# Optimization experiments

Measured on AMD Instinct MI355X. Metric: run time of the kernel, lower is better.

## Reference

```python
import jax, jax.numpy as jnp
import numpy as np

B, T, N, F = 32, 24, 1024, 2   # batch, seq_len, num_adj, num_feature
HID = 32                       # opt['hidden_dim']
U = HID // 2                   # rnn_units = 16
TF = 31                        # opt['time_feature']


def setup_inputs():
    key = jax.random.key(0)
    ks = jax.random.split(key, 40)
    def nrm(k, shape):
        return jax.random.normal(k, shape, dtype=jnp.float32) * 0.05
    inp = {}
    inp['recent_data'] = nrm(ks[0], (B, T, N, F))
    inp['trend_data'] = nrm(ks[1], (B, T, F))
    # normalized adjacency-like matrix (non-negative, row mass ~1)
    inp['sub_graph'] = jax.random.uniform(ks[2], (B, N, N), dtype=jnp.float32) * (2.0 / N)
    inp['time_feature'] = nrm(ks[3], (B, TF))
    i = 4
    for layer, insz in ((1, F + U), (2, U + U)):
        for g in 'ruc':
            inp[f'gru{layer}_{g}W'] = nrm(ks[i], (U, insz)); i += 1
            inp[f'gru{layer}_{g}b'] = jnp.zeros((U,), jnp.float32)
    for l, insz in ((0, F), (1, HID)):
        inp[f'lstm_Wih{l}'] = nrm(ks[i], (4 * HID, insz)); i += 1
        inp[f'lstm_Whh{l}'] = nrm(ks[i], (4 * HID, HID)); i += 1
        inp[f'lstm_bih{l}'] = jnp.zeros((4 * HID,), jnp.float32)
        inp[f'lstm_bhh{l}'] = jnp.zeros((4 * HID,), jnp.float32)
    inp['ff_W'] = nrm(ks[i], (HID, TF)); i += 1
    inp['ff_b'] = jnp.zeros((HID,), jnp.float32)
    inp['gcn_W'] = nrm(ks[i], (F, int(HID * 2.5))); i += 1
    inp['gcn_b'] = jnp.zeros((F,), jnp.float32)
    return inp


def _gcn(x, A, W, b, act):
    # x: (B,N,in), A: (B,N,N) -> act(fc(A @ x)): (B,N,out)
    return act(jnp.einsum('bij,bjf->bif', A, x) @ W.T + b)


def _gru_cell(x, h, A, rW, rb, uW, ub, cW, cb):
    xh = jnp.concatenate([x, h], axis=-1)
    r = _gcn(xh, A, rW, rb, jax.nn.sigmoid)
    u = _gcn(xh, A, uW, ub, jax.nn.sigmoid)
    c = _gcn(jnp.concatenate([x, r * h], axis=-1), A, cW, cb, jnp.tanh)
    return u * h + (1.0 - u) * c


def _lstm_layer(xs, Wih, Whh, bih, bhh):
    # xs: (T, B, in) -> hidden sequence (T, B, H); PyTorch gate order i,f,g,o
    H = Whh.shape[1]
    z = jnp.zeros((xs.shape[1], H), xs.dtype)
    def step(carry, x_t):
        h, c = carry
        g = x_t @ Wih.T + h @ Whh.T + bih + bhh
        i, f, gg, o = jnp.split(g, 4, axis=-1)
        c = jax.nn.sigmoid(f) * c + jax.nn.sigmoid(i) * jnp.tanh(gg)
        h = jax.nn.sigmoid(o) * jnp.tanh(c)
        return (h, c), h
    _, hs = jax.lax.scan(step, (z, z), xs)
    return hs


def _forward(recent_data, trend_data, sub_graph, time_feature,
             gru1_rW, gru1_rb, gru1_uW, gru1_ub, gru1_cW, gru1_cb,
             gru2_rW, gru2_rb, gru2_uW, gru2_ub, gru2_cW, gru2_cb,
             lstm_Wih0, lstm_Whh0, lstm_bih0, lstm_bhh0,
             lstm_Wih1, lstm_Whh1, lstm_bih1, lstm_bhh1,
             ff_W, ff_b, gcn_W, gcn_b):
    b, t, n, _ = recent_data.shape
    u = gru1_rW.shape[0]
    h0 = jnp.zeros((b, n, u), recent_data.dtype)
    # 2-layer GCGRU encoder over time (only final output/state is used)
    def step(carry, x_t):
        h1, h2 = carry
        h1 = _gru_cell(x_t, h1, sub_graph, gru1_rW, gru1_rb, gru1_uW, gru1_ub, gru1_cW, gru1_cb)
        h2 = _gru_cell(h1, h2, sub_graph, gru2_rW, gru2_rb, gru2_uW, gru2_ub, gru2_cW, gru2_cb)
        return (h1, h2), None
    (h1, h2), _ = jax.lax.scan(step, (h0, h0), jnp.swapaxes(recent_data, 0, 1))
    recent = h2  # (B, N, U)
    # 2-layer LSTM on trend_data; take last timestep hidden
    xs = jnp.swapaxes(trend_data, 0, 1)  # (T, B, F)
    hs = _lstm_layer(xs, lstm_Wih0, lstm_Whh0, lstm_bih0, lstm_bhh0)
    hs = _lstm_layer(hs, lstm_Wih1, lstm_Whh1, lstm_bih1, lstm_bhh1)
    trend = jnp.broadcast_to(hs[-1][:, None, :], (b, n, hs.shape[-1]))
    feat = jax.nn.relu(time_feature @ ff_W.T + ff_b)
    feat = jnp.broadcast_to(feat[:, None, :], (b, n, feat.shape[-1]))
    combined = jnp.concatenate([recent, trend, feat], axis=-1)  # (B, N, 2.5*HID)
    return _gcn(combined, sub_graph, gcn_W, gcn_b, jnp.tanh)  # (B, N, F)


def reference(recent_data, trend_data, sub_graph, time_feature,
              gru1_rW, gru1_rb, gru1_uW, gru1_ub, gru1_cW, gru1_cb,
              gru2_rW, gru2_rb, gru2_uW, gru2_ub, gru2_cW, gru2_cb,
              lstm_Wih0, lstm_Whh0, lstm_bih0, lstm_bhh0,
              lstm_Wih1, lstm_Whh1, lstm_bih1, lstm_bhh1,
              ff_W, ff_b, gcn_W, gcn_b):
    return _forward(recent_data, trend_data, sub_graph, time_feature,
                    gru1_rW, gru1_rb, gru1_uW, gru1_ub, gru1_cW, gru1_cb,
                    gru2_rW, gru2_rb, gru2_uW, gru2_ub, gru2_cW, gru2_cb,
                    lstm_Wih0, lstm_Whh0, lstm_bih0, lstm_bhh0,
                    lstm_Wih1, lstm_Whh1, lstm_bih1, lstm_bhh1,
                    ff_W, ff_b, gcn_W, gcn_b)
```

## Files before the change

### kernel.cpp

```cpp
#include <hip/hip_runtime.h>
#include <cmath>
#include <stdint.h>

#define BB 32
#define TT 24
#define NN 1024
#define FF 2
#define UU 16
#define HH 32
#define TFN 31
#define NWG 256

typedef __attribute__((ext_vector_type(8))) short bf16x8;
typedef __attribute__((ext_vector_type(4))) float f32x4;
typedef unsigned short u16;
typedef unsigned int   u32;
typedef __attribute__((ext_vector_type(4))) u32 u32x4;

#define RU1A 0
#define RU1B 32
#define C1R  64
#define RU2R 80
#define C2R  112
__device__ __align__(16) u16 g_Y[BB][128*NN];
__device__ float g_c2[BB*FF];
__device__ __align__(256) u32 g_bar[BB][64];
__device__ u32 g_xcdmask[BB];

__device__ __forceinline__ float sigmf(float x){ return 1.f/(1.f+expf(-x)); }
__device__ __forceinline__ u16 f2bf(float f){
  u32 u = __float_as_uint(f);
  return (u16)((u + 0x7fffu + ((u>>16)&1u)) >> 16);
}
__device__ __forceinline__ void ywr(u16* Yb, int j, int n, float s, bool modeA){
  u16* p = (u16*)((char*)Yb + (j<<11) + (((n<<1)) ^ ((j&7)<<4)));
  u16 v = f2bf(s);
  if (modeA) *p = v;
  else __hip_atomic_store(p, v, __ATOMIC_RELAXED, __HIP_MEMORY_SCOPE_AGENT);
}

__device__ __forceinline__ void bbar(u32* cnt, u32 target){
  __syncthreads();
  if (threadIdx.x == 0){
    u32 old = __hip_atomic_fetch_add(cnt, 1u, __ATOMIC_RELAXED, __HIP_MEMORY_SCOPE_AGENT);
    if (old + 1u < target){
      for (u32 it=0; it<200000u; ++it){
        if (__hip_atomic_load(cnt, __ATOMIC_RELAXED, __HIP_MEMORY_SCOPE_AGENT) >= target)
          break;
        if (it < 4) __builtin_amdgcn_s_sleep(1);
        else        __builtin_amdgcn_s_sleep(4);
      }
    }
  }
  __syncthreads();
}

template<int W>
__device__ __forceinline__ void stageY(const u16* __restrict__ Yb, u16* Ys,
                                       int tid, bool modeA){
  u32x4 r[W/4];
  if (modeA){
#pragma unroll
    for (int q=0;q<W/4;q++){
      const char* src = (const char*)Yb + q*8192 + tid*16;
      asm volatile("global_load_dwordx4 %0, %1, off sc0"
                   : "=v"(r[q]) : "v"(src));
    }
  } else {
#pragma unroll
    for (int q=0;q<W/4;q++){
      const char* src = (const char*)Yb + q*8192 + tid*16;
      asm volatile("global_load_dwordx4 %0, %1, off sc0 sc1"
                   : "=v"(r[q]) : "v"(src));
    }
  }
  asm volatile("s_waitcnt vmcnt(0)" ::: "memory");
  __builtin_amdgcn_sched_barrier(0);
#pragma unroll
  for (int q=0;q<W/4;q++)
    *(u32x4*)((char*)Ys + q*8192 + tid*16) = r[q];
}

__device__ __forceinline__ void mm32(const bf16x8 (&areg)[32], const u16* Ys,
                                     int base0, int cflip, f32x4& a0, f32x4& a1){
#pragma unroll
  for (int c=0;c<32;c++){
    int off = base0 + ((c ^ cflip) << 6);
    bf16x8 b0 = *(const bf16x8*)((const char*)Ys + off);
    bf16x8 b1 = *(const bf16x8*)((const char*)Ys + off + 32768);
    a0 = __builtin_amdgcn_mfma_f32_16x16x32_bf16(areg[c], b0, a0, 0, 0, 0);
    a1 = __builtin_amdgcn_mfma_f32_16x16x32_bf16(areg[c], b1, a1, 0, 0, 0);
  }
}
__device__ __forceinline__ void mm16(const bf16x8 (&areg)[32], const u16* Ys,
                                     int base0, int cflip, f32x4& a0){
#pragma unroll
  for (int c=0;c<32;c++){
    int off = base0 + ((c ^ cflip) << 6);
    bf16x8 b0 = *(const bf16x8*)((const char*)Ys + off);
    a0 = __builtin_amdgcn_mfma_f32_16x16x32_bf16(areg[c], b0, a0, 0, 0, 0);
  }
}

__global__ __launch_bounds__(128)
void k_lstm(const float* __restrict__ trend, const float* __restrict__ tfeat,
            const float* __restrict__ Wih0, const float* __restrict__ Whh0,
            const float* __restrict__ bih0, const float* __restrict__ bhh0,
            const float* __restrict__ Wih1, const float* __restrict__ Whh1,
            const float* __restrict__ bih1, const float* __restrict__ bhh1,
            const float* __restrict__ ffW, const float* __restrict__ ffb,
            const float* __restrict__ gcnW) {
  __shared__ float h[HH], c[HH], g[4*HH], hs0[TT][HH], tr[HH], fe[HH];
  int b = blockIdx.x, tid = threadIdx.x;
  if (tid == 0){
    __hip_atomic_store(&g_bar[b][0],  0u, __ATOMIC_RELAXED, __HIP_MEMORY_SCOPE_AGENT);
    __hip_atomic_store(&g_xcdmask[b], 0u, __ATOMIC_RELAXED, __HIP_MEMORY_SCOPE_AGENT);
  }
  if (tid < HH) { h[tid]=0.f; c[tid]=0.f; }
  __syncthreads();
  for (int t=0;t<TT;t++) {
    float x0 = trend[(b*TT+t)*FF+0], x1 = trend[(b*TT+t)*FF+1];
    float gv = bih0[tid] + bhh0[tid] + x0*Wih0[tid*FF+0] + x1*Wih0[tid*FF+1];
#pragma unroll
    for (int k=0;k<HH;k++) gv += h[k]*Whh0[tid*HH+k];
    g[tid] = gv;
    __syncthreads();
    if (tid < HH) {
      float ii = sigmf(g[tid]), ff = sigmf(g[HH+tid]);
      float gg = tanhf(g[2*HH+tid]), oo = sigmf(g[3*HH+tid]);
      float cn = ff*c[tid] + ii*gg;
      c[tid] = cn;
      float hn = oo*tanhf(cn);
      h[tid] = hn;
      hs0[t][tid] = hn;
    }
    __syncthreads();
  }
  if (tid < HH) { h[tid]=0.f; c[tid]=0.f; }
  __syncthreads();
  for (int t=0;t<TT;t++) {
    float gv = bih1[tid] + bhh1[tid];
#pragma unroll
    for (int k=0;k<HH;k++) gv += hs0[t][k]*Wih1[tid*HH+k];
#pragma unroll
    for (int k=0;k<HH;k++) gv += h[k]*Whh1[tid*HH+k];
    g[tid] = gv;
    __syncthreads();
    if (tid < HH) {
      float ii = sigmf(g[tid]), ff = sigmf(g[HH+tid]);
      float gg = tanhf(g[2*HH+tid]), oo = sigmf(g[3*HH+tid]);
      float cn = ff*c[tid] + ii*gg;
      c[tid] = cn;
      h[tid] = oo*tanhf(cn);
    }
    __syncthreads();
  }
  if (tid < HH) {
    tr[tid] = h[tid];
    float fv = ffb[tid];
#pragma unroll
    for (int j=0;j<TFN;j++) fv += tfeat[b*TFN+j]*ffW[tid*TFN+j];
    fe[tid] = fmaxf(fv, 0.f);
  }
  __syncthreads();
  if (tid < FF) {
    float s = 0.f;
#pragma unroll
    for (int j=0;j<HH;j++) s += tr[j]*gcnW[tid*80+16+j];
#pragma unroll
    for (int j=0;j<HH;j++) s += fe[j]*gcnW[tid*80+48+j];
    g_c2[b*FF+tid] = s;
  }
}

struct KP {
  const float *recent, *A;
  const float *g1rW,*g1rb,*g1uW,*g1ub,*g1cW,*g1cb;
  const float *g2rW,*g2rb,*g2uW,*g2ub,*g2cW,*g2cb;
  const float *gcnW,*gcnb;
  float *out;
};

__global__ __launch_bounds__(512, 2)
void k_main(KP p){
  __shared__ __align__(16) u16 Ys[32*NN];
  __shared__ float Ps [128][33];
  __shared__ float h1s[128][17];
  __shared__ float h2s[128][17];
  __shared__ float us_[128][17];
  __shared__ float rhs[128][17];

  const int wg = blockIdx.x;
  const int b = (wg & 7)*4 + (wg >> 6);
  const int i0 = ((wg >> 3) & 7) << 7;
  const int tid = threadIdx.x;
  const int v = tid >> 6, lane = tid & 63, m = lane & 15, quad = lane >> 4;
  const int rloc = v << 4;
  const int row = tid >> 2, jj = tid & 3;
  const int n = i0 + row;
  const int base0 = m*2048 + ((quad ^ (m & 3)) << 4);
  const int cflip = (m >> 2) & 1;
  u32* bar = &g_bar[b][0];
  u16* Yb  = &g_Y[b][0];

  if (tid == 0){
    u32 xcc;
    asm volatile("s_getreg_b32 %0, hwreg(HW_REG_XCC_ID)" : "=s"(xcc));
    u32 oldm = __hip_atomic_fetch_or(&g_xcdmask[b], 1u << (xcc & 31),
                                     __ATOMIC_RELAXED, __HIP_MEMORY_SCOPE_AGENT);
    asm volatile("" :: "v"(oldm));
  }

  bf16x8 areg[32];
  {
    const float* Ab = p.A + ((size_t)(b*NN + i0 + rloc + m))*NN + quad*8;
#pragma unroll
    for (int c=0;c<32;c++){
      float4 f0 = *(const float4*)(Ab + c*32);
      float4 f1 = *(const float4*)(Ab + c*32 + 4);
      bf16x8 tv;
      tv[0]=(short)f2bf(f0.x); tv[1]=(short)f2bf(f0.y);
      tv[2]=(short)f2bf(f0.z); tv[3]=(short)f2bf(f0.w);
      tv[4]=(short)f2bf(f1.x); tv[5]=(short)f2bf(f1.y);
      tv[6]=(short)f2bf(f1.z); tv[7]=(short)f2bf(f1.w);
      areg[c] = tv;
    }
  }

#pragma unroll
  for (int q=0;q<4;q++){ h1s[row][jj*4+q]=0.f; h2s[row][jj*4+q]=0.f; }

  {
    const float* xr = p.recent + (((size_t)b*TT)*NN + n)*FF;
    float x0 = xr[0], x1 = xr[1];
    u16* Yr = Yb + RU1A*NN;
#pragma unroll
    for (int m2=0;m2<8;m2++){
      int j = jj*8 + m2;
      const float* W = (j<16) ? (p.g1rW + j*18) : (p.g1uW + (j-16)*18);
      ywr(Yr, j, n, x0*W[0] + x1*W[1], false);
    }
  }
  u32 gen = 0;
  bbar(bar, (++gen)*8);

  const u32 mk = __hip_atomic_load(&g_xcdmask[b], __ATOMIC_RELAXED,
                                   __HIP_MEMORY_SCOPE_AGENT);
  const bool modeA = (__popc(mk) == 1);

  for (int t=0;t<TT;t++){
    stageY<32>(Yb + ((t&1) ? RU1B : RU1A)*NN, Ys, tid, modeA);
    __syncthreads();
    {
      f32x4 a0={0.f,0.f,0.f,0.f}, a1={0.f,0.f,0.f,0.f};
      mm32(areg, Ys, base0, cflip, a0, a1);
#pragma unroll
      for (int r=0;r<4;r++){
        Ps[rloc + quad*4 + r][m]    = a0[r];
        Ps[rloc + quad*4 + r][16+m] = a1[r];
      }
    }
    __syncthreads();
#pragma unroll
    for (int q=0;q<4;q++){
      int j = jj*4+q;
      float rv = sigmf(Ps[row][j]    + p.g1rb[j]);
      float uv = sigmf(Ps[row][16+j] + p.g1ub[j]);
      us_[row][j] = uv;
      rhs[row][j] = rv * h1s[row][j];
    }
    __syncthreads();
    {
      const float* xr = p.recent + (((size_t)b*TT + t)*NN + n)*FF;
      float x0 = xr[0], x1 = xr[1];
      u16* Yc = Yb + C1R*NN;
#pragma unroll
      for (int q=0;q<4;q++){
        int j = jj*4+q;
        const float* W = p.g1cW + j*18;
        float s = fmaf(x0, W[0], x1*W[1]);
#pragma unroll
        for (int f=0;f<16;f++) s = fmaf(rhs[row][f], W[2+f], s);
        ywr(Yc, j, n, s, modeA);
      }
    }
    bbar(bar, (++gen)*8);

    stageY<16>(Yb + C1R*NN, Ys, tid, modeA);
    __syncthreads();
    {
      f32x4 a0={0.f,0.f,0.f,0.f};
      mm16(areg, Ys, base0, cflip, a0);
#pragma unroll
      for (int r=0;r<4;r++) Ps[rloc + quad*4 + r][m] = a0[r];
    }
    __syncthreads();
#pragma unroll
    for (int q=0;q<4;q++){
      int j = jj*4+q;
      float cv = tanhf(Ps[row][j] + p.g1cb[j]);
      float uv = us_[row][j];
      h1s[row][j] = uv*h1s[row][j] + (1.f-uv)*cv;
    }
    __syncthreads();
    {
      u16* Yr2 = Yb + RU2R*NN;
#pragma unroll
      for (int m2=0;m2<8;m2++){
        int j = jj*8 + m2;
        const float* W = (j<16) ? (p.g2rW + j*32) : (p.g2uW + (j-16)*32);
        float s = 0.f;
#pragma unroll
        for (int f=0;f<16;f++) s = fmaf(h1s[row][f], W[f],    s);
#pragma unroll
        for (int f=0;f<16;f++) s = fmaf(h2s[row][f], W[16+f], s);
        ywr(Yr2, j, n, s, modeA);
      }
      if (t < TT-1){
        const float* xr = p.recent + (((size_t)b*TT + t + 1)*NN + n)*FF;
        float x0 = xr[0], x1 = xr[1];
        u16* Yr1 = Yb + (((t+1)&1) ? RU1B : RU1A)*NN;
#pragma unroll
        for (int m2=0;m2<8;m2++){
          int j = jj*8 + m2;
          const float* W = (j<16) ? (p.g1rW + j*18) : (p.g1uW + (j-16)*18);
          float s = fmaf(x0, W[0], x1*W[1]);
#pragma unroll
          for (int f=0;f<16;f++) s = fmaf(h1s[row][f], W[2+f], s);
          ywr(Yr1, j, n, s, modeA);
        }
      }
    }
    bbar(bar, (++gen)*8);

    stageY<32>(Yb + RU2R*NN, Ys, tid, modeA);
    __syncthreads();
    {
      f32x4 a0={0.f,0.f,0.f,0.f}, a1={0.f,0.f,0.f,0.f};
      mm32(areg, Ys, base0, cflip, a0, a1);
#pragma unroll
      for (int r=0;r<4;r++){
        Ps[rloc + quad*4 + r][m]    = a0[r];
        Ps[rloc + quad*4 + r][16+m] = a1[r];
      }
    }
    __syncthreads();
#pragma unroll
    for (int q=0;q<4;q++){
      int j = jj*4+q;
      float rv = sigmf(Ps[row][j]    + p.g2rb[j]);
      float uv = sigmf(Ps[row][16+j] + p.g2ub[j]);
      us_[row][j] = uv;
      rhs[row][j] = rv * h2s[row][j];
    }
    __syncthreads();
    {
      u16* Yc2 = Yb + C2R*NN;
#pragma unroll
      for (int q=0;q<4;q++){
        int j = jj*4+q;
        const float* W = p.g2cW + j*32;
        float s = 0.f;
#pragma unroll
        for (int f=0;f<16;f++) s = fmaf(h1s[row][f], W[f],    s);
#pragma unroll
        for (int f=0;f<16;f++) s = fmaf(rhs[row][f], W[16+f], s);
        ywr(Yc2, j, n, s, modeA);
      }
    }
    bbar(bar, (++gen)*8);

    stageY<16>(Yb + C2R*NN, Ys, tid, modeA);
    __syncthreads();
    {
      f32x4 a0={0.f,0.f,0.f,0.f};
      mm16(areg, Ys, base0, cflip, a0);
#pragma unroll
      for (int r=0;r<4;r++) Ps[rloc + quad*4 + r][m] = a0[r];
    }
    __syncthreads();
#pragma unroll
    for (int q=0;q<4;q++){
      int j = jj*4+q;
      float cv = tanhf(Ps[row][j] + p.g2cb[j]);
      float uv = us_[row][j];
      h2s[row][j] = uv*h2s[row][j] + (1.f-uv)*cv;
    }
    __syncthreads();
    if (t == TT-1){
      u16* Yc = Yb + C1R*NN;
#pragma unroll
      for (int q=0;q<4;q++){
        int j = jj*4+q;
        float s = 0.f;
        if (j < FF){
          s = g_c2[b*FF + j];
#pragma unroll
          for (int f=0;f<16;f++) s = fmaf(h2s[row][f], p.gcnW[j*80+f], s);
        }
        ywr(Yc, j, n, s, modeA);
      }
      bbar(bar, (++gen)*8);
    }
  }

  stageY<16>(Yb + C1R*NN, Ys, tid, modeA);
  __syncthreads();
  {
    f32x4 a0={0.f,0.f,0.f,0.f};
    mm16(areg, Ys, base0, cflip, a0);
    if (m < FF){
      float bb = p.gcnb[m];
#pragma unroll
      for (int r=0;r<4;r++){
        int nn = i0 + rloc + quad*4 + r;
        p.out[((size_t)b*NN + nn)*FF + m] = tanhf(a0[r] + bb);
      }
    }
  }
}

extern "C" void kernel_launch(void* const* d_in, const int* in_sizes, int n_in,
                              void* d_out, int out_size, void* d_ws, size_t ws_size,
                              hipStream_t stream) {
  (void)in_sizes; (void)n_in; (void)d_ws; (void)ws_size; (void)out_size;
  const float* recent = (const float*)d_in[0];
  const float* trend  = (const float*)d_in[1];
  const float* A      = (const float*)d_in[2];
  const float* tfeat  = (const float*)d_in[3];
  const float* g1rW = (const float*)d_in[4];  const float* g1rb = (const float*)d_in[5];
  const float* g1uW = (const float*)d_in[6];  const float* g1ub = (const float*)d_in[7];
  const float* g1cW = (const float*)d_in[8];  const float* g1cb = (const float*)d_in[9];
  const float* g2rW = (const float*)d_in[10]; const float* g2rb = (const float*)d_in[11];
  const float* g2uW = (const float*)d_in[12]; const float* g2ub = (const float*)d_in[13];
  const float* g2cW = (const float*)d_in[14]; const float* g2cb = (const float*)d_in[15];
  const float* Wih0 = (const float*)d_in[16]; const float* Whh0 = (const float*)d_in[17];
  const float* bih0 = (const float*)d_in[18]; const float* bhh0 = (const float*)d_in[19];
  const float* Wih1 = (const float*)d_in[20]; const float* Whh1 = (const float*)d_in[21];
  const float* bih1 = (const float*)d_in[22]; const float* bhh1 = (const float*)d_in[23];
  const float* ffW  = (const float*)d_in[24]; const float* ffb  = (const float*)d_in[25];
  const float* gcnW = (const float*)d_in[26]; const float* gcnb = (const float*)d_in[27];
  float* out = (float*)d_out;

  k_lstm<<<BB, 128, 0, stream>>>(trend, tfeat, Wih0, Whh0, bih0, bhh0,
                                 Wih1, Whh1, bih1, bhh1, ffW, ffb, gcnW);

  KP kp;
  kp.recent = recent; kp.A = A;
  kp.g1rW=g1rW; kp.g1rb=g1rb; kp.g1uW=g1uW; kp.g1ub=g1ub; kp.g1cW=g1cW; kp.g1cb=g1cb;
  kp.g2rW=g2rW; kp.g2rb=g2rb; kp.g2uW=g2uW; kp.g2ub=g2ub; kp.g2cW=g2cW; kp.g2cb=g2cb;
  kp.gcnW=gcnW; kp.gcnb=gcnb; kp.out=out;
  void* args[] = { (void*)&kp };
  hipLaunchCooperativeKernel((const void*)k_main, dim3(NWG), dim3(512), args, 0, stream);
}
```

Before: 1.638 ms.

## Assign batches dynamically per XCD and replace counter barrier with per-slot flags

```diff
diff --git a/kernel.cpp b/kernel.cpp
--- a/kernel.cpp
+++ b/kernel.cpp
@@ -24,55 +24,43 @@
 #define C2R  112
 __device__ __align__(16) u16 g_Y[BB][128*NN];
 __device__ float g_c2[BB*FF];
-__device__ __align__(256) u32 g_bar[BB][64];
-__device__ u32 g_xcdmask[BB];
+__device__ __align__(256) u32 g_fl[BB][8][64];
+__device__ __align__(256) u32 g_slot[8][64];
 
 __device__ __forceinline__ float sigmf(float x){ return 1.f/(1.f+expf(-x)); }
 __device__ __forceinline__ u16 f2bf(float f){
   u32 u = __float_as_uint(f);
   return (u16)((u + 0x7fffu + ((u>>16)&1u)) >> 16);
 }
-__device__ __forceinline__ void ywr(u16* Yb, int j, int n, float s, bool modeA){
-  u16* p = (u16*)((char*)Yb + (j<<11) + (((n<<1)) ^ ((j&7)<<4)));
-  u16 v = f2bf(s);
-  if (modeA) *p = v;
-  else __hip_atomic_store(p, v, __ATOMIC_RELAXED, __HIP_MEMORY_SCOPE_AGENT);
-}
-
-__device__ __forceinline__ void bbar(u32* cnt, u32 target){
-  __syncthreads();
-  if (threadIdx.x == 0){
-    u32 old = __hip_atomic_fetch_add(cnt, 1u, __ATOMIC_RELAXED, __HIP_MEMORY_SCOPE_AGENT);
-    if (old + 1u < target){
-      for (u32 it=0; it<200000u; ++it){
-        if (__hip_atomic_load(cnt, __ATOMIC_RELAXED, __HIP_MEMORY_SCOPE_AGENT) >= target)
-          break;
-        if (it < 4) __builtin_amdgcn_s_sleep(1);
-        else        __builtin_amdgcn_s_sleep(4);
-      }
+__device__ __forceinline__ void ywr(u16* Yb, int j, int n, float s){
+  *(u16*)((char*)Yb + (j<<11) + (((n<<1)) ^ ((j&7)<<4))) = f2bf(s);
+}
+
+__device__ __forceinline__ void sigwait(u32* myfl, const u32* flb, u32 want, int tid){
+  __syncthreads();
+  if (tid == 0)
+    __hip_atomic_store(myfl, want, __ATOMIC_RELAXED, __HIP_MEMORY_SCOPE_AGENT);
+  if (tid < 64){
+    const u32* p = flb + (tid & 7)*64;
+    for (u32 it=0; it<50000u; ++it){
+      u32 v;
+      asm volatile("global_load_dword %0, %1, off sc0 sc1\n\t"
+                   "s_waitcnt vmcnt(0)" : "=v"(v) : "v"(p) : "memory");
+      if (__all((int)(v >= want))) break;
+      __builtin_amdgcn_s_sleep(1);
     }
   }
   __syncthreads();
 }
 
 template<int W>
-__device__ __forceinline__ void stageY(const u16* __restrict__ Yb, u16* Ys,
-                                       int tid, bool modeA){
+__device__ __forceinline__ void stageY(const u16* __restrict__ Yb, u16* Ys, int tid){
   u32x4 r[W/4];
-  if (modeA){
-#pragma unroll
-    for (int q=0;q<W/4;q++){
-      const char* src = (const char*)Yb + q*8192 + tid*16;
-      asm volatile("global_load_dwordx4 %0, %1, off sc0"
-                   : "=v"(r[q]) : "v"(src));
-    }
-  } else {
-#pragma unroll
-    for (int q=0;q<W/4;q++){
-      const char* src = (const char*)Yb + q*8192 + tid*16;
-      asm volatile("global_load_dwordx4 %0, %1, off sc0 sc1"
-                   : "=v"(r[q]) : "v"(src));
-    }
+#pragma unroll
+  for (int q=0;q<W/4;q++){
+    const char* src = (const char*)Yb + q*8192 + tid*16;
+    asm volatile("global_load_dwordx4 %0, %1, off sc0"
+                 : "=v"(r[q]) : "v"(src));
   }
   asm volatile("s_waitcnt vmcnt(0)" ::: "memory");
   __builtin_amdgcn_sched_barrier(0);
@@ -112,10 +100,10 @@
             const float* __restrict__ gcnW) {
   __shared__ float h[HH], c[HH], g[4*HH], hs0[TT][HH], tr[HH], fe[HH];
   int b = blockIdx.x, tid = threadIdx.x;
-  if (tid == 0){
-    __hip_atomic_store(&g_bar[b][0],  0u, __ATOMIC_RELAXED, __HIP_MEMORY_SCOPE_AGENT);
-    __hip_atomic_store(&g_xcdmask[b], 0u, __ATOMIC_RELAXED, __HIP_MEMORY_SCOPE_AGENT);
-  }
+  if (tid < 8)
+    __hip_atomic_store(&g_fl[b][tid][0], 0u, __ATOMIC_RELAXED, __HIP_MEMORY_SCOPE_AGENT);
+  if (b == 0 && tid < 8)
+    __hip_atomic_store(&g_slot[tid][0], 0u, __ATOMIC_RELAXED, __HIP_MEMORY_SCOPE_AGENT);
   if (tid < HH) { h[tid]=0.f; c[tid]=0.f; }
   __syncthreads();
   for (int t=0;t<TT;t++) {
@@ -189,27 +177,30 @@
   __shared__ float h2s[128][17];
   __shared__ float us_[128][17];
   __shared__ float rhs[128][17];
-
-  const int wg = blockIdx.x;
-  const int b = (wg & 7)*4 + (wg >> 6);
-  const int i0 = ((wg >> 3) & 7) << 7;
+  __shared__ int sb, sg;
+
   const int tid = threadIdx.x;
+  if (tid == 0){
+    u32 xcc;
+    asm volatile("s_getreg_b32 %0, hwreg(HW_REG_XCC_ID)" : "=s"(xcc));
+    xcc &= 7u;
+    u32 s = __hip_atomic_fetch_add(&g_slot[xcc][0], 1u,
+                                   __ATOMIC_RELAXED, __HIP_MEMORY_SCOPE_AGENT);
+    sb = (int)(xcc*4u + (s >> 3));
+    sg = (int)(s & 7u);
+  }
+  __syncthreads();
+  const int b = sb, gslot = sg;
+  const int i0 = gslot << 7;
   const int v = tid >> 6, lane = tid & 63, m = lane & 15, quad = lane >> 4;
   const int rloc = v << 4;
   const int row = tid >> 2, jj = tid & 3;
   const int n = i0 + row;
   const int base0 = m*2048 + ((quad ^ (m & 3)) << 4);
   const int cflip = (m >> 2) & 1;
-  u32* bar = &g_bar[b][0];
-  u16* Yb  = &g_Y[b][0];
-
-  if (tid == 0){
-    u32 xcc;
-    asm volatile("s_getreg_b32 %0, hwreg(HW_REG_XCC_ID)" : "=s"(xcc));
-    u32 oldm = __hip_atomic_fetch_or(&g_xcdmask[b], 1u << (xcc & 31),
-                                     __ATOMIC_RELAXED, __HIP_MEMORY_SCOPE_AGENT);
-    asm volatile("" :: "v"(oldm));
-  }
+  u16* Yb   = &g_Y[b][0];
+  u32* flb  = &g_fl[b][0][0];
+  u32* myfl = &g_fl[b][gslot][0];
 
   bf16x8 areg[32];
   {
@@ -238,18 +229,14 @@
     for (int m2=0;m2<8;m2++){
       int j = jj*8 + m2;
       const float* W = (j<16) ? (p.g1rW + j*18) : (p.g1uW + (j-16)*18);
-      ywr(Yr, j, n, x0*W[0] + x1*W[1], false);
+      ywr(Yr, j, n, x0*W[0] + x1*W[1]);
     }
   }
   u32 gen = 0;
-  bbar(bar, (++gen)*8);
-
-  const u32 mk = __hip_atomic_load(&g_xcdmask[b], __ATOMIC_RELAXED,
-                                   __HIP_MEMORY_SCOPE_AGENT);
-  const bool modeA = (__popc(mk) == 1);
+  sigwait(myfl, flb, ++gen, tid);
 
   for (int t=0;t<TT;t++){
-    stageY<32>(Yb + ((t&1) ? RU1B : RU1A)*NN, Ys, tid, modeA);
+    stageY<32>(Yb + ((t&1) ? RU1B : RU1A)*NN, Ys, tid);
     __syncthreads();
     {
       f32x4 a0={0.f,0.f,0.f,0.f}, a1={0.f,0.f,0.f,0.f};
@@ -281,12 +268,12 @@
         float s = fmaf(x0, W[0], x1*W[1]);
 #pragma unroll
         for (int f=0;f<16;f++) s = fmaf(rhs[row][f], W[2+f], s);
-        ywr(Yc, j, n, s, modeA);
-      }
-    }
-    bbar(bar, (++gen)*8);
-
-    stageY<16>(Yb + C1R*NN, Ys, tid, modeA);
+        ywr(Yc, j, n, s);
+      }
+    }
+    sigwait(myfl, flb, ++gen, tid);
+
+    stageY<16>(Yb + C1R*NN, Ys, tid);
     __syncthreads();
     {
       f32x4 a0={0.f,0.f,0.f,0.f};
@@ -314,7 +301,7 @@
         for (int f=0;f<16;f++) s = fmaf(h1s[row][f], W[f],    s);
 #pragma unroll
         for (int f=0;f<16;f++) s = fmaf(h2s[row][f], W[16+f], s);
-        ywr(Yr2, j, n, s, modeA);
+        ywr(Yr2, j, n, s);
       }
       if (t < TT-1){
         const float* xr = p.recent + (((size_t)b*TT + t + 1)*NN + n)*FF;
@@ -327,13 +314,13 @@
           float s = fmaf(x0, W[0], x1*W[1]);
 #pragma unroll
           for (int f=0;f<16;f++) s = fmaf(h1s[row][f], W[2+f], s);
-          ywr(Yr1, j, n, s, modeA);
+          ywr(Yr1, j, n, s);
         }
       }
     }
-    bbar(bar, (++gen)*8);
-
-    stageY<32>(Yb + RU2R*NN, Ys, tid, modeA);
+    sigwait(myfl, flb, ++gen, tid);
+
+    stageY<32>(Yb + RU2R*NN, Ys, tid);
     __syncthreads();
     {
       f32x4 a0={0.f,0.f,0.f,0.f}, a1={0.f,0.f,0.f,0.f};
@@ -365,12 +352,12 @@
         for (int f=0;f<16;f++) s = fmaf(h1s[row][f], W[f],    s);
 #pragma unroll
         for (int f=0;f<16;f++) s = fmaf(rhs[row][f], W[16+f], s);
-        ywr(Yc2, j, n, s, modeA);
-      }
-    }
-    bbar(bar, (++gen)*8);
-
-    stageY<16>(Yb + C2R*NN, Ys, tid, modeA);
+        ywr(Yc2, j, n, s);
+      }
+    }
+    sigwait(myfl, flb, ++gen, tid);
+
+    stageY<16>(Yb + C2R*NN, Ys, tid);
     __syncthreads();
     {
       f32x4 a0={0.f,0.f,0.f,0.f};
@@ -398,13 +385,13 @@
 #pragma unroll
           for (int f=0;f<16;f++) s = fmaf(h2s[row][f], p.gcnW[j*80+f], s);
         }
-        ywr(Yc, j, n, s, modeA);
-      }
-      bbar(bar, (++gen)*8);
-    }
-  }
-
-  stageY<16>(Yb + C1R*NN, Ys, tid, modeA);
+        ywr(Yc, j, n, s);
+      }
+      sigwait(myfl, flb, ++gen, tid);
+    }
+  }
+
+  stageY<16>(Yb + C1R*NN, Ys, tid);
   __syncthreads();
   {
     f32x4 a0={0.f,0.f,0.f,0.f};
```

New measurement: 2.112 ms. +29.0%, slower.
